# Performance work log

Measured on AMD Instinct MI355X. Metric: run time of the kernel, lower is better.

## Reference

```python
import math
import jax, jax.numpy as jnp
import numpy as np

N_HEADS = 16
HEAD_DIM = 128
NUM_BUCKETS = 32
MAX_DISTANCE = 128
ROPE_BASE = 10000.0


def _rope_cos_sin(seq_len, head_dim, dtype):
    inv_freq = 1.0 / (ROPE_BASE ** (jnp.arange(0, head_dim, 2, dtype=jnp.float32) / head_dim))
    ang = jnp.arange(seq_len, dtype=jnp.float32)[:, None] * inv_freq[None, :]  # [S, hd/2]
    return jnp.cos(ang).astype(dtype), jnp.sin(ang).astype(dtype)


def _apply_rope(t, cos, sin):
    # t: [B, S, H, D] (NeoX rotate-half); cos/sin: [S, D/2]
    d2 = t.shape[-1] // 2
    t1, t2 = t[..., :d2], t[..., d2:]
    c = cos[None, :, None, :]
    s = sin[None, :, None, :]
    return jnp.concatenate([t1 * c - t2 * s, t2 * c + t1 * s], axis=-1)


def _relative_bucket(q_len, k_len):
    # unidirectional (causal) T5 bucketing: relative_position = 0 - min(mem - ctx, 0)
    ctx = jnp.arange(q_len, dtype=jnp.int32)[:, None]
    mem = jnp.arange(k_len, dtype=jnp.int32)[None, :]
    n = jnp.maximum(ctx - mem, 0)  # [Q, K]
    max_exact = NUM_BUCKETS // 2
    is_small = n < max_exact
    nf = jnp.maximum(n, 1).astype(jnp.float32)
    large = (jnp.log(nf / max_exact) / math.log(MAX_DISTANCE / max_exact)
             * (NUM_BUCKETS - max_exact)).astype(jnp.int32) + max_exact
    large = jnp.minimum(large, NUM_BUCKETS - 1)
    return jnp.where(is_small, n, large)


def setup_inputs() -> dict:
    key = jax.random.key(0)
    k1, k2, k3, k4 = jax.random.split(key, 4)
    B, S, H = 2, 2048, 2048
    return {
        "x": jax.random.normal(k1, (B, S, H), jnp.float32),
        "qkv_w": jax.random.normal(k2, (H, 3 * H), jnp.float32) * 0.02,
        "dense_w": jax.random.normal(k3, (H, H), jnp.float32) * 0.02,
        "rel_attn_table": jax.random.normal(k4, (NUM_BUCKETS, N_HEADS), jnp.float32) * 0.1,
    }


def reference(x, qkv_w, dense_w, rel_attn_table):
    B, S, H = x.shape
    qkv = x @ qkv_w                         # [B, S, 3H]
    q, k, v = jnp.split(qkv, 3, axis=-1)
    q = q.reshape(B, S, N_HEADS, HEAD_DIM)
    k = k.reshape(B, S, N_HEADS, HEAD_DIM)
    v = v.reshape(B, S, N_HEADS, HEAD_DIM)

    cos, sin = _rope_cos_sin(S, HEAD_DIM, x.dtype)
    q = _apply_rope(q, cos, sin)
    k = _apply_rope(k, cos, sin)

    scale = 1.0 / math.sqrt(HEAD_DIM)       # q_scaling = 1.0
    scores = jnp.einsum("bqhd,bkhd->bhqk", q, k) * scale  # [B, nH, S, S]

    # T5 relative position bias: embedding(bucket, table).permute(2,0,1) -> [1, nH, S, S]
    bucket = _relative_bucket(S, S)
    bias = rel_attn_table[bucket]            # [S, S, nH]
    scores = scores + jnp.transpose(bias, (2, 0, 1))[None]

    # causal mask (make_causal_mask): key index > query index -> large negative
    causal = jnp.tril(jnp.ones((S, S), dtype=bool))
    neg = jnp.asarray(jnp.finfo(x.dtype).min, x.dtype)
    scores = jnp.where(causal[None, None], scores, neg)

    probs = jax.nn.softmax(scores, axis=-1)
    ctx = jnp.einsum("bhqk,bkhd->bqhd", probs, v).reshape(B, S, H)
    return ctx @ dense_w
```

## Files before the change

kernel.cpp:

```cpp
#include <hip/hip_runtime.h>

typedef unsigned short u16;
typedef __bf16 bf16_t;
typedef __bf16 bf16x8 __attribute__((ext_vector_type(8)));
typedef float f32x4 __attribute__((ext_vector_type(4)));
typedef unsigned short u16x8 __attribute__((ext_vector_type(8)));
typedef unsigned short u16x4 __attribute__((ext_vector_type(4)));

#define S_LEN 2048
#define NHEAD 16
#define HD 128
#define HID 2048
#define QKV_N 6144

__device__ __forceinline__ float b2f(u16 u) {
  union { unsigned int i; float f; } x; x.i = ((unsigned int)u) << 16; return x.f;
}
__device__ __forceinline__ u16 f2b(float f) {
  bf16_t h = (bf16_t)f;
  return __builtin_bit_cast(unsigned short, h);
}

__device__ __forceinline__ void gl_lds16(const u16* g, u16* l) {
  __builtin_amdgcn_global_load_lds(
      (const __attribute__((address_space(1))) unsigned int*)g,
      (__attribute__((address_space(3))) unsigned int*)l, 16, 0, 0);
}

__global__ void detect_dtype_k(const void* __restrict__ x, int* __restrict__ flag) {
  __shared__ int cnt;
  if (threadIdx.x == 0) cnt = 0;
  __syncthreads();
  const u16* xu = (const u16*)x;
  int sane = 0;
  for (int i = threadIdx.x; i < 8192; i += 256) {
    int e = (xu[i] >> 7) & 0xFF;
    if (e == 0 || (e > 100 && e < 140)) sane++;
  }
  atomicAdd(&cnt, sane);
  __syncthreads();
  if (threadIdx.x == 0) *flag = (cnt < 7373) ? 1 : 0;
}

__global__ __launch_bounds__(256) void convert_any_k(const void* __restrict__ in, u16* __restrict__ out,
                                                     const int* __restrict__ flag) {
  int i = (blockIdx.x * 256 + threadIdx.x) * 4;
  if (*flag) {
    const float4 v = *(const float4*)((const float*)in + i);
    u16x4 o = {f2b(v.x), f2b(v.y), f2b(v.z), f2b(v.w)};
    *(u16x4*)(out + i) = o;
  } else {
    *(u16x4*)(out + i) = *(const u16x4*)((const u16*)in + i);
  }
}

__global__ __launch_bounds__(256) void transpose_any(const void* __restrict__ in,
                                                     u16* __restrict__ out, int R, int C,
                                                     const int* __restrict__ flag) {
  __shared__ u16 t[64][65];
  bool isf = (*flag != 0);
  int tid = threadIdx.x;
  int r0 = blockIdx.y * 64, c0 = blockIdx.x * 64;
#pragma unroll
  for (int p = 0; p < 16; ++p) {
    int e = p * 256 + tid;
    int r = e >> 6, c = e & 63;
    size_t idx = (size_t)(r0 + r) * C + (c0 + c);
    t[r][c] = isf ? f2b(((const float*)in)[idx]) : ((const u16*)in)[idx];
  }
  __syncthreads();
#pragma unroll
  for (int p = 0; p < 16; ++p) {
    int e = p * 256 + tid;
    int r = e >> 6, c = e & 63;
    out[(size_t)(c0 + r) * R + (r0 + c)] = t[c][r];
  }
}

__global__ void rope_table_k(float* __restrict__ tab) {
  int i = blockIdx.x * 256 + threadIdx.x;
  int s = i >> 6, d = i & 63;
  float inv = expf(-(float)d * (9.210340371976184f / 64.0f));
  float ang = (float)s * inv;
  tab[s * 128 + d] = cosf(ang);
  tab[s * 128 + 64 + d] = sinf(ang);
}

__global__ void build_bias_k(const void* __restrict__ table, float* __restrict__ bias,
                             const int* __restrict__ flag) {
  int i = blockIdx.x * 256 + threadIdx.x;
  int h = i >> 11, dist = i & 2047;
  int bucket;
  if (dist < 16) bucket = dist;
  else {
    int lb = (int)(logf((float)dist * 0.0625f) / 2.0794415f * 16.0f) + 16;
    bucket = lb < 31 ? lb : 31;
  }
  int ti = bucket * NHEAD + h;
  float tv = (*flag) ? ((const float*)table)[ti] : b2f(((const u16*)table)[ti]);
  bias[h * 2048 + dist] = tv;
}

template <bool F32OUT>
__global__ __launch_bounds__(512, 2) void gemm128_bt(const u16* __restrict__ A,
                                                     const u16* __restrict__ B,
                                                     void* __restrict__ Cv,
                                                     int M, int N, int K) {
  __shared__ __align__(16) u16 sA[2][8192];
  __shared__ __align__(16) u16 sB[2][16384];
  (void)M;
  const int tid = threadIdx.x;
  const int lane = tid & 63, w = tid >> 6;
  const int wm = w >> 2, wn = w & 3;
  const int lane16 = lane & 15, quad = lane >> 4;

  const int nbx = gridDim.x;
  const int nwg = nbx * gridDim.y;
  const int bid = blockIdx.y * nbx + blockIdx.x;
  const int cpx = nwg >> 3;
  const int swz = (bid & 7) * cpx + (bid >> 3);
  const int m0 = (swz / nbx) * 128;
  const int n0 = (swz % nbx) * 256;

  const int rl = lane >> 2;
  const int ch = (lane & 3) ^ (((lane >> 5) & 1) << 1);
  const u16* pA_ = A + (size_t)(m0 + w * 16 + rl) * K + ch * 8;
  const u16* pB_ = B + (size_t)(n0 + w * 16 + rl) * K + ch * 8;

  const int fro = lane16 * 32 + ((quad * 8) ^ ((lane16 & 8) << 1));

  f32x4 zero4 = {0.f, 0.f, 0.f, 0.f};
  f32x4 acc[4][4];
#pragma unroll
  for (int i = 0; i < 4; ++i)
#pragma unroll
    for (int j = 0; j < 4; ++j) acc[i][j] = zero4;

  bf16x8 a0[2][2], a1[2][2];
  bf16x8 Bf[4][2];

#define STAGE_A(BUF, KO)                                         \
  do {                                                           \
    const u16* _s = pA_ + (KO);                                  \
    u16* _d = &sA[BUF][w * 1024];                                \
    gl_lds16(_s, _d);                                            \
    gl_lds16(_s + 32, _d + 512);                                 \
  } while (0)
#define STAGE_B(BUF, H, KO)                                      \
  do {                                                           \
    const u16* _s = pB_ + (size_t)(H) * 128 * K + (KO);          \
    u16* _d = &sB[BUF][(H) * 8192 + w * 1024];                   \
    gl_lds16(_s, _d);                                            \
    gl_lds16(_s + 32, _d + 512);                                 \
  } while (0)
#define READ_A(DST, BUF, MH)                                                         \
  _Pragma("unroll") for (int i = 0; i < 2; ++i)                                      \
  _Pragma("unroll") for (int ks = 0; ks < 2; ++ks)                                   \
    DST[i][ks] = *(const bf16x8*)&sA[BUF][((wm * 4 + (MH) * 2 + i) * 2 + ks) * 512 + fro];
#define READ_BF(BUF)                                                                 \
  _Pragma("unroll") for (int j = 0; j < 4; ++j)                                      \
  _Pragma("unroll") for (int ks = 0; ks < 2; ++ks)                                   \
    Bf[j][ks] = *(const bf16x8*)&sB[BUF][((wn * 4 + j) * 2 + ks) * 512 + fro];
#define MFMA_H(AF, MH)                                                               \
  __builtin_amdgcn_s_setprio(1);                                                     \
  _Pragma("unroll") for (int i = 0; i < 2; ++i)                                      \
  _Pragma("unroll") for (int j = 0; j < 4; ++j)                                      \
  _Pragma("unroll") for (int ks = 0; ks < 2; ++ks)                                   \
    acc[(MH) * 2 + i][j] = __builtin_amdgcn_mfma_f32_16x16x32_bf16(                  \
        AF[i][ks], Bf[j][ks], acc[(MH) * 2 + i][j], 0, 0, 0);                        \
  __builtin_amdgcn_s_setprio(0);
#define GBAR() __builtin_amdgcn_s_barrier()
#define VMCNT4() asm volatile("s_waitcnt vmcnt(4)" ::: "memory")
#define VMCNT6() asm volatile("s_waitcnt vmcnt(6)" ::: "memory")

  STAGE_B(0, 0, 0); STAGE_B(0, 1, 0); STAGE_A(0, 0);
  STAGE_B(1, 0, 64); STAGE_B(1, 1, 64); STAGE_A(1, 64);
  VMCNT6();
  GBAR();
  READ_A(a0, 0, 0); READ_BF(0);

  const int nIt = K >> 7;
  for (int it = 0; it < nIt; ++it) {
    int base = it << 7;
    int k2 = base + 128; if (k2 >= K) k2 = 0;
    int k3 = base + 192; if (k3 >= K) k3 = 0;
    GBAR();
    MFMA_H(a0, 0);
    STAGE_B(0, 0, k2); STAGE_B(0, 1, k2);
    READ_A(a1, 0, 1);
    VMCNT4();
    GBAR();
    MFMA_H(a1, 1);
    STAGE_A(0, k2);
    READ_BF(1); READ_A(a0, 1, 0);
    GBAR();
    MFMA_H(a0, 0);
    STAGE_B(1, 0, k3); STAGE_B(1, 1, k3);
    READ_A(a1, 1, 1);
    VMCNT4();
    GBAR();
    MFMA_H(a1, 1);
    STAGE_A(1, k3);
    READ_BF(0); READ_A(a0, 0, 0);
  }
  asm volatile("s_waitcnt vmcnt(0)" ::: "memory");

#pragma unroll
  for (int i = 0; i < 4; ++i)
#pragma unroll
    for (int j = 0; j < 4; ++j)
#pragma unroll
      for (int r = 0; r < 4; ++r) {
        int row = m0 + wm * 64 + i * 16 + quad * 4 + r;
        int col = n0 + wn * 64 + j * 16 + lane16;
        if (F32OUT)
          ((float*)Cv)[(size_t)row * N + col] = acc[i][j][r];
        else
          ((u16*)Cv)[(size_t)row * N + col] = f2b(acc[i][j][r]);
      }
#undef STAGE_A
#undef STAGE_B
#undef READ_A
#undef READ_BF
#undef MFMA_H
#undef GBAR
#undef VMCNT4
#undef VMCNT6
}

__global__ __launch_bounds__(256) void reorg_k(const u16* __restrict__ qkv, const float* __restrict__ tab,
                                               u16* __restrict__ q, u16* __restrict__ k,
                                               u16* __restrict__ vT) {
  __shared__ float vt[64][129];
  int tid = threadIdx.x;
  int st = blockIdx.x, bh = blockIdx.y;
  int b = bh >> 4, h = bh & 15;
  int s0 = st * 64;
  const u16* base = qkv + (size_t)(b * S_LEN + s0) * QKV_N + h * HD;
  u16* qo = q + ((size_t)bh * S_LEN + s0) * HD;
  u16* ko = k + ((size_t)bh * S_LEN + s0) * HD;
#pragma unroll
  for (int p = 0; p < 16; ++p) {
    int e = p * 256 + tid;
    int sl = e >> 6, d = e & 63;
    float c = tab[(s0 + sl) * 128 + d];
    float sn = tab[(s0 + sl) * 128 + 64 + d];
    const u16* rowp = base + (size_t)sl * QKV_N;
    float q1 = b2f(rowp[d]), q2 = b2f(rowp[d + 64]);
    qo[sl * HD + d] = f2b(q1 * c - q2 * sn);
    qo[sl * HD + d + 64] = f2b(q2 * c + q1 * sn);
    float k1 = b2f(rowp[2048 + d]), k2 = b2f(rowp[2048 + d + 64]);
    ko[sl * HD + d] = f2b(k1 * c - k2 * sn);
    ko[sl * HD + d + 64] = f2b(k2 * c + k1 * sn);
  }
#pragma unroll
  for (int p = 0; p < 32; ++p) {
    int e = p * 256 + tid;
    int sl = e >> 7, d = e & 127;
    vt[sl][d] = b2f(base[(size_t)sl * QKV_N + 4096 + d]);
  }
  __syncthreads();
  u16* vo = vT + (size_t)bh * HD * S_LEN;
#pragma unroll
  for (int p = 0; p < 32; ++p) {
    int e = p * 256 + tid;
    int d = e >> 6, sl = e & 63;
    vo[(size_t)d * S_LEN + s0 + sl] = f2b(vt[sl][d]);
  }
}

__global__ __launch_bounds__(256) void attn_k(const u16* __restrict__ q, const u16* __restrict__ k,
                                              const u16* __restrict__ vT, const float* __restrict__ bias,
                                              u16* __restrict__ ctx) {
  __shared__ __align__(16) u16 Ks[64 * 128];
  __shared__ __align__(16) u16 VTs[128 * 64];
  __shared__ __align__(16) u16 QP[64 * 128];
  __shared__ float bias_s[128];
  int tid = threadIdx.x;
  int lane = tid & 63, wq = tid >> 6;
  int lane16 = lane & 15, quad = lane >> 4;
  int r7 = lane16 & 7;
  int bh = blockIdx.y;
  int b = bh >> 4, h = bh & 15;
  const u16* kg = k + (size_t)bh * S_LEN * HD;
  const u16* vg = vT + (size_t)bh * HD * S_LEN;
  const float* biasr = bias + h * 2048;
  const float scale = 0.08838834764831845f;
  f32x4 zero4 = {0.f, 0.f, 0.f, 0.f};

  int rl4 = lane >> 4, pk = lane & 15;
  int rl8 = lane >> 3, pv = lane & 7;
  u16* Pw = QP + wq * 1152;

  for (int half = 0; half < 2; ++half) {
    int qt = half ? (31 - blockIdx.x) : blockIdx.x;
    int q0 = qt * 64;
    const u16* qg = q + ((size_t)bh * S_LEN + q0) * HD;

    __syncthreads();
    {
      int r = tid >> 4, c = (tid & 15) * 8;
#pragma unroll
      for (int p = 0; p < 4; ++p)
        *(u16x8*)&QP[(r + p * 16) * 128 + c] = *(const u16x8*)&qg[(size_t)(r + p * 16) * HD + c];
    }
    __syncthreads();
    bf16x8 qf[4];
#pragma unroll
    for (int kd = 0; kd < 4; ++kd)
      qf[kd] = *(const bf16x8*)&QP[(wq * 16 + lane16) * 128 + kd * 32 + quad * 8];
    __syncthreads();

    float m_i[4], l_i[4];
    f32x4 o[8];
#pragma unroll
    for (int r = 0; r < 4; ++r) { m_i[r] = -1e30f; l_i[r] = 0.f; }
#pragma unroll
    for (int dt = 0; dt < 8; ++dt) o[dt] = zero4;

    for (int kt = 0; kt <= qt; ++kt) {
      int k0 = kt * 64;
      if (kt) __syncthreads();
#pragma unroll
      for (int t = 0; t < 4; ++t) {
        int g = wq * 4 + t;
        int rowk = g * 4 + rl4;
        int ck = (pk & 8) | ((pk & 7) ^ (rowk & 7));
        gl_lds16(kg + (size_t)(k0 + rowk) * HD + ck * 8, Ks + g * 512);
        int rowv = g * 8 + rl8;
        int cv = pv ^ (rowv & 7);
        gl_lds16(vg + (size_t)rowv * S_LEN + k0 + cv * 8, VTs + g * 512);
      }
      if (tid < 128) {
        int dist = q0 - k0 + tid - 64;
        bias_s[tid] = (dist >= 0) ? biasr[dist] : 0.f;
      }
      __syncthreads();

      f32x4 sc[4];
#pragma unroll
      for (int j = 0; j < 4; ++j) sc[j] = zero4;
#pragma unroll
      for (int kd = 0; kd < 4; ++kd)
#pragma unroll
        for (int j = 0; j < 4; ++j) {
          int cd = kd * 4 + quad;
          int pos = (cd & 8) | ((cd & 7) ^ r7);
          bf16x8 kf = *(const bf16x8*)&Ks[(j * 16 + lane16) * 128 + pos * 8];
          sc[j] = __builtin_amdgcn_mfma_f32_16x16x32_bf16(qf[kd], kf, sc[j], 0, 0, 0);
        }

      int qrel = wq * 16 + quad * 4;
#pragma unroll
      for (int j = 0; j < 4; ++j) {
        int krel = j * 16 + lane16;
#pragma unroll
        for (int r = 0; r < 4; ++r) {
          bool valid = (q0 + qrel + r) >= (k0 + krel);
          float sv = sc[j][r] * scale + bias_s[64 + (qrel + r) - krel];
          sc[j][r] = valid ? sv : -1e30f;
        }
      }
      float mx[4];
#pragma unroll
      for (int r = 0; r < 4; ++r)
        mx[r] = fmaxf(fmaxf(sc[0][r], sc[1][r]), fmaxf(sc[2][r], sc[3][r]));
#pragma unroll
      for (int xm = 1; xm < 16; xm <<= 1)
#pragma unroll
        for (int r = 0; r < 4; ++r) mx[r] = fmaxf(mx[r], __shfl_xor(mx[r], xm));
      float alpha[4];
#pragma unroll
      for (int r = 0; r < 4; ++r) {
        float mn = fmaxf(m_i[r], mx[r]);
        alpha[r] = __expf(m_i[r] - mn);
        m_i[r] = mn;
      }
#pragma unroll
      for (int j = 0; j < 4; ++j)
#pragma unroll
        for (int r = 0; r < 4; ++r) sc[j][r] = __expf(sc[j][r] - m_i[r]);
      float rs[4];
#pragma unroll
      for (int r = 0; r < 4; ++r) rs[r] = (sc[0][r] + sc[1][r]) + (sc[2][r] + sc[3][r]);
#pragma unroll
      for (int xm = 1; xm < 16; xm <<= 1)
#pragma unroll
        for (int r = 0; r < 4; ++r) rs[r] += __shfl_xor(rs[r], xm);
#pragma unroll
      for (int r = 0; r < 4; ++r) l_i[r] = l_i[r] * alpha[r] + rs[r];
#pragma unroll
      for (int dt = 0; dt < 8; ++dt)
#pragma unroll
        for (int r = 0; r < 4; ++r) o[dt][r] *= alpha[r];

#pragma unroll
      for (int j = 0; j < 4; ++j)
#pragma unroll
        for (int r = 0; r < 4; ++r)
          Pw[(quad * 4 + r) * 72 + j * 16 + lane16] = f2b(sc[j][r]);
      __threadfence_block();

#pragma unroll
      for (int ks = 0; ks < 2; ++ks) {
        bf16x8 pf = *(const bf16x8*)&Pw[lane16 * 72 + ks * 32 + quad * 8];
#pragma unroll
        for (int dt = 0; dt < 8; ++dt) {
          int cdv = ks * 4 + quad;
          int posv = cdv ^ r7;
          bf16x8 vf = *(const bf16x8*)&VTs[(dt * 16 + lane16) * 64 + posv * 8];
          o[dt] = __builtin_amdgcn_mfma_f32_16x16x32_bf16(pf, vf, o[dt], 0, 0, 0);
        }
      }
    }
#pragma unroll
    for (int r = 0; r < 4; ++r) {
      float invl = 1.0f / l_i[r];
      int srow = q0 + wq * 16 + quad * 4 + r;
      u16* orow = ctx + ((size_t)b * S_LEN + srow) * HID + h * HD;
#pragma unroll
      for (int dt = 0; dt < 8; ++dt)
        orow[dt * 16 + lane16] = f2b(o[dt][r] * invl);
    }
  }
}

extern "C" void kernel_launch(void* const* d_in, const int* in_sizes, int n_in,
                              void* d_out, int out_size, void* d_ws, size_t ws_size,
                              hipStream_t stream) {
  const void* x       = d_in[0];
  const void* qkv_w   = d_in[1];
  const void* dense_w = d_in[2];
  const void* rtable  = d_in[3];
  char* ws = (char*)d_ws;

  int*   flag  = (int*)(ws);
  float* bias  = (float*)(ws + 256);
  float* tab   = (float*)(ws + 131328);
  u16*   wdT   = (u16*)(ws + 1179904);
  u16*   vT    = (u16*)(ws + 9568512);
  u16*   x_bf  = (u16*)(ws + 26345728);
  u16*   qA    = x_bf;
  u16*   wqkvT = (u16*)(ws + 43122944);
  u16*   kA    = wqkvT;
  u16*   qkv   = (u16*)(ws + 68288768);
  u16*   ctx   = qkv;

  detect_dtype_k<<<1, 256, 0, stream>>>(x, flag);
  convert_any_k<<<8192, 256, 0, stream>>>(x, x_bf, flag);
  transpose_any<<<dim3(96, 32), 256, 0, stream>>>(qkv_w, wqkvT, 2048, 6144, flag);
  transpose_any<<<dim3(32, 32), 256, 0, stream>>>(dense_w, wdT, 2048, 2048, flag);
  rope_table_k<<<512, 256, 0, stream>>>(tab);
  build_bias_k<<<128, 256, 0, stream>>>(rtable, bias, flag);
  gemm128_bt<false><<<dim3(24, 32), 512, 0, stream>>>(x_bf, wqkvT, qkv, 4096, 6144, 2048);
  reorg_k<<<dim3(32, 32), 256, 0, stream>>>(qkv, tab, qA, kA, vT);
  attn_k<<<dim3(16, 32), 256, 0, stream>>>(qA, kA, vT, bias, ctx);
  gemm128_bt<true><<<dim3(8, 32), 512, 0, stream>>>(ctx, wdT, d_out, 4096, 2048, 2048);
}
```

Before: 466.9 us.

## Use 256x256 tiled GEMM kernel for QKV projection

Adds a gemm256_bt kernel that computes a 256x256 output tile per workgroup, with a quadrant-wise MFMA schedule interleaved with double-buffered global-to-LDS staging. The QKV projection switches to it, which halves the grid and doubles operand reuse per tile, cutting global and LDS traffic per FLOP. In exchange it uses more accumulator registers (128 floats per lane) and more shared memory, which may lower occupancy or cause spills. The 384-block grid is also small relative to the CU count, so wave quantization may hurt.

```diff
diff --git a/kernel.cpp b/kernel.cpp
--- a/kernel.cpp
+++ b/kernel.cpp
@@ -99,6 +99,135 @@
   int ti = bucket * NHEAD + h;
   float tv = (*flag) ? ((const float*)table)[ti] : b2f(((const u16*)table)[ti]);
   bias[h * 2048 + dist] = tv;
+}
+
+template <bool F32OUT>
+__global__ __launch_bounds__(512, 2) void gemm256_bt(const u16* __restrict__ A,
+                                                     const u16* __restrict__ B,
+                                                     void* __restrict__ Cv,
+                                                     int M, int N, int K) {
+  __shared__ __align__(16) u16 sA[2][16384];
+  __shared__ __align__(16) u16 sB[2][16384];
+  (void)M;
+  const int tid = threadIdx.x;
+  const int lane = tid & 63, w = tid >> 6;
+  const int wm = w >> 2, wn = w & 3;
+  const int lane16 = lane & 15, quad = lane >> 4;
+
+  const int nbx = gridDim.x;
+  const int nwg = nbx * gridDim.y;
+  const int bid = blockIdx.y * nbx + blockIdx.x;
+  const int cpx = nwg >> 3;
+  const int swz = (bid & 7) * cpx + (bid >> 3);
+  const int m0 = (swz / nbx) * 256;
+  const int n0 = (swz % nbx) * 256;
+
+  const int rl = lane >> 2;
+  const int ch = (lane & 3) ^ (((lane >> 5) & 1) << 1);
+  const u16* pA_ = A + (size_t)(m0 + w * 16 + rl) * K + ch * 8;
+  const u16* pB_ = B + (size_t)(n0 + w * 16 + rl) * K + ch * 8;
+
+  const int fro = lane16 * 32 + ((quad * 8) ^ ((lane16 & 8) << 1));
+
+  f32x4 zero4 = {0.f, 0.f, 0.f, 0.f};
+  f32x4 acc[8][4];
+#pragma unroll
+  for (int i = 0; i < 8; ++i)
+#pragma unroll
+    for (int j = 0; j < 4; ++j) acc[i][j] = zero4;
+
+  bf16x8 a0[4][2], a1[4][2];
+  bf16x8 b0[2][2], b1[2][2];
+
+#define STAGE_A(BUF, H, KO)                                      \
+  do {                                                           \
+    const u16* _s = pA_ + (size_t)(H) * 128 * K + (KO);          \
+    u16* _d = &sA[BUF][(H) * 8192 + w * 1024];                   \
+    gl_lds16(_s, _d);                                            \
+    gl_lds16(_s + 32, _d + 512);                                 \
+  } while (0)
+#define STAGE_B(BUF, H, KO)                                      \
+  do {                                                           \
+    const u16* _s = pB_ + (size_t)(H) * 128 * K + (KO);          \
+    u16* _d = &sB[BUF][(H) * 8192 + w * 1024];                   \
+    gl_lds16(_s, _d);                                            \
+    gl_lds16(_s + 32, _d + 512);                                 \
+  } while (0)
+#define READ_A(DST, BUF, MH)                                                         \
+  _Pragma("unroll") for (int i = 0; i < 4; ++i)                                      \
+  _Pragma("unroll") for (int ks = 0; ks < 2; ++ks)                                   \
+    DST[i][ks] = *(const bf16x8*)&sA[BUF][((wm * 8 + (MH) * 4 + i) * 2 + ks) * 512 + fro];
+#define READ_B(DST, BUF, NH)                                                         \
+  _Pragma("unroll") for (int j = 0; j < 2; ++j)                                      \
+  _Pragma("unroll") for (int ks = 0; ks < 2; ++ks)                                   \
+    DST[j][ks] = *(const bf16x8*)&sB[BUF][((wn * 4 + (NH) * 2 + j) * 2 + ks) * 512 + fro];
+#define MFMA_Q(AF, BF, MH, NH)                                                       \
+  __builtin_amdgcn_s_setprio(1);                                                     \
+  _Pragma("unroll") for (int i = 0; i < 4; ++i)                                      \
+  _Pragma("unroll") for (int j = 0; j < 2; ++j)                                      \
+  _Pragma("unroll") for (int ks = 0; ks < 2; ++ks)                                   \
+    acc[(MH) * 4 + i][(NH) * 2 + j] = __builtin_amdgcn_mfma_f32_16x16x32_bf16(       \
+        AF[i][ks], BF[j][ks], acc[(MH) * 4 + i][(NH) * 2 + j], 0, 0, 0);             \
+  __builtin_amdgcn_s_setprio(0);
+#define GBAR() __builtin_amdgcn_s_barrier()
+#define VMCNT8() asm volatile("s_waitcnt vmcnt(8)" ::: "memory")
+
+  STAGE_A(0, 0, 0); STAGE_A(0, 1, 0);
+  STAGE_B(0, 0, 0); STAGE_B(0, 1, 0);
+  STAGE_B(1, 0, 64); STAGE_B(1, 1, 64);
+  STAGE_A(1, 0, 64); STAGE_A(1, 1, 64);
+  VMCNT8();
+  GBAR();
+  READ_A(a0, 0, 0); READ_B(b0, 0, 0);
+
+  const int nIt = K >> 7;
+  for (int it = 0; it < nIt; ++it) {
+    int base = it << 7;
+    int k2 = base + 128; if (k2 >= K) k2 = 0;
+    int k3 = base + 192; if (k3 >= K) k3 = 0;
+    GBAR(); MFMA_Q(a0, b0, 0, 0);
+    READ_B(b1, 0, 1);
+    GBAR(); MFMA_Q(a0, b1, 0, 1);
+    READ_A(a1, 0, 1);
+    STAGE_B(0, 0, k2); STAGE_B(0, 1, k2);
+    GBAR(); MFMA_Q(a1, b1, 1, 1);
+    STAGE_A(0, 0, k2); STAGE_A(0, 1, k2);
+    VMCNT8();
+    GBAR(); MFMA_Q(a1, b0, 1, 0);
+    READ_A(a0, 1, 0); READ_B(b0, 1, 0);
+    GBAR(); MFMA_Q(a0, b0, 0, 0);
+    READ_B(b1, 1, 1);
+    GBAR(); MFMA_Q(a0, b1, 0, 1);
+    READ_A(a1, 1, 1);
+    STAGE_B(1, 0, k3); STAGE_B(1, 1, k3);
+    GBAR(); MFMA_Q(a1, b1, 1, 1);
+    STAGE_A(1, 0, k3); STAGE_A(1, 1, k3);
+    VMCNT8();
+    GBAR(); MFMA_Q(a1, b0, 1, 0);
+    READ_A(a0, 0, 0); READ_B(b0, 0, 0);
+  }
+  asm volatile("s_waitcnt vmcnt(0)" ::: "memory");
+
+#pragma unroll
+  for (int i = 0; i < 8; ++i)
+#pragma unroll
+    for (int j = 0; j < 4; ++j)
+#pragma unroll
+      for (int r = 0; r < 4; ++r) {
+        int row = m0 + wm * 128 + i * 16 + quad * 4 + r;
+        int col = n0 + wn * 64 + j * 16 + lane16;
+        if (F32OUT)
+          ((float*)Cv)[(size_t)row * N + col] = acc[i][j][r];
+        else
+          ((u16*)Cv)[(size_t)row * N + col] = f2b(acc[i][j][r]);
+      }
+#undef STAGE_A
+#undef STAGE_B
+#undef READ_A
+#undef READ_B
+#undef MFMA_Q
+#undef GBAR
+#undef VMCNT8
 }
 
 template <bool F32OUT>
@@ -452,7 +581,7 @@
   transpose_any<<<dim3(32, 32), 256, 0, stream>>>(dense_w, wdT, 2048, 2048, flag);
   rope_table_k<<<512, 256, 0, stream>>>(tab);
   build_bias_k<<<128, 256, 0, stream>>>(rtable, bias, flag);
-  gemm128_bt<false><<<dim3(24, 32), 512, 0, stream>>>(x_bf, wqkvT, qkv, 4096, 6144, 2048);
+  gemm256_bt<false><<<dim3(24, 16), 512, 0, stream>>>(x_bf, wqkvT, qkv, 4096, 6144, 2048);
   reorg_k<<<dim3(32, 32), 256, 0, stream>>>(qkv, tab, qA, kA, vT);
   attn_k<<<dim3(16, 32), 256, 0, stream>>>(qA, kA, vT, bias, ctx);
   gemm128_bt<true><<<dim3(8, 32), 512, 0, stream>>>(ctx, wdT, d_out, 4096, 2048, 2048);
```

Measured after the change: 433.7 us. 7.1% less time.
